# Optimization experiments

Measured on AMD Instinct MI355X. Metric: run time of the kernel, lower is better.

## Reference

```python
import jax, jax.numpy as jnp
import numpy as np
from jax import lax

SHIFT = 32  # shift_range from init
EPS_NORM = 1e-12
EPS_MASK = 1e-6


def _l2_normalize_flat(x):
    # F.normalize(x.reshape(B,-1)): per-sample L2 normalize with eps 1e-12
    B = x.shape[0]
    flat = x.reshape(B, -1)
    n = jnp.linalg.norm(flat, axis=1, keepdims=True)
    return (flat / jnp.maximum(n, EPS_NORM)).reshape(x.shape)


def setup_inputs() -> dict:
    key = jax.random.key(0)
    k1, k2 = jax.random.split(key)
    grd_feature = jax.random.normal(k1, (8, 32, 32, 32), dtype=jnp.float32)
    sat_feature = jax.random.normal(k2, (8, 32, 128, 128), dtype=jnp.float32)
    return {"grd_feature": grd_feature, "sat_feature": sat_feature, "test_method": 1}


def reference(grd_feature, sat_feature, test_method):
    # test_method == 1 path (default); test_method in {0,1} only differ in divisor
    M, C, H_s, W_s = sat_feature.shape
    N, _, H, W = grd_feature.shape
    kH = min(H, H_s - 2 * SHIFT)
    kW = min(W, W_s - 2 * SHIFT)

    # center-crop ground template to (kH, kW) and L2-normalize per sample
    gh0, gw0 = H // 2 - kH // 2, W // 2 - kW // 2
    grd = grd_feature[:, :, gh0:gh0 + 2 * (kH // 2), gw0:gw0 + 2 * (kW // 2)]
    N_, _, H_k, W_k = grd.shape
    grd = _l2_normalize_flat(grd)

    # center-crop satellite to search region and L2-normalize per sample
    sh0 = H_s // 2 - SHIFT - kH // 2
    sw0 = W_s // 2 - SHIFT - kW // 2
    sat = sat_feature[:, :, sh0:sh0 + 2 * (SHIFT + kH // 2), sw0:sw0 + 2 * (SHIFT + kW // 2)]
    _, _, H_i, W_i = sat.shape
    sat = _l2_normalize_flat(sat)

    # all-pairs cross-correlation: corr[m, n, y, x] (torch grouped-conv on repeated sat
    # is equivalent to a plain VALID conv of sat with all N ground filters)
    corr = lax.conv_general_dilated(
        sat, grd, window_strides=(1, 1), padding='VALID',
        dimension_numbers=('NCHW', 'OIHW', 'NCHW'))  # [M, N, Ho, Wo]
    Ho, Wo = corr.shape[2], corr.shape[3]

    # sliding-window sum of |sat|^2 (avg_pool with divisor_override=1, summed over C)
    s2 = jnp.sum(sat * sat, axis=1)  # [M, H_i, W_i]
    partical = lax.reduce_window(s2, jnp.float32(0), lax.add,
                                 (1, H_k, W_k), (1, 1, 1), 'VALID')  # [M, Ho, Wo]
    if test_method == 0:
        denom = jnp.sqrt(partical)
    else:
        denom = partical
    corr = corr / jnp.maximum(denom[:, None], EPS_NORM)

    similarity_matrix = jnp.max(corr, axis=(2, 3))  # [M, N]

    # diagonal pairs (m == n): peak localization
    diag = jnp.diagonal(corr, axis1=0, axis2=1)        # [Ho, Wo, M]
    diag = jnp.transpose(diag, (2, 0, 1)).reshape(M, -1)
    max_index = jnp.argmax(diag, axis=-1)
    pos_h = max_index // Wo
    pos_w = max_index % Wo

    grd_mask = (jnp.abs(jnp.sum(grd, axis=1)) > EPS_MASK).astype(jnp.float32)  # [N, H_k, W_k]

    def place(ph, pw, gm):
        z = jnp.zeros((1, H_i, W_i), dtype=jnp.float32)
        return lax.dynamic_update_slice(z, gm[None], (0, ph, pw))

    mask = jax.vmap(place)(pos_h, pos_w, grd_mask)  # [M, 1, H_i, W_i]
    return similarity_matrix, mask
```

## Files before the change

### kernel.cpp

```cpp
#include <hip/hip_runtime.h>
#include <stdint.h>

typedef unsigned short u16;
typedef unsigned int u32;
typedef unsigned long long u64;
typedef __bf16 bf16x8 __attribute__((ext_vector_type(8)));
typedef float floatx4 __attribute__((ext_vector_type(4)));

#define DEVI static __device__ __forceinline__

DEVI u16 f2bf(float f) {
  uint32_t u = __builtin_bit_cast(uint32_t, f);
  u += 0x7FFFu + ((u >> 16) & 1u);
  return (u16)(u >> 16);
}
DEVI float bf2f(u16 b) { return __builtin_bit_cast(float, (uint32_t)b << 16); }

DEVI u32 encf(float f) {
  u32 u = __builtin_bit_cast(u32, f);
  return (u >> 31) ? ~u : (u | 0x80000000u);
}

DEVI float wred_sum(float v) {
  #pragma unroll
  for (int o = 32; o > 0; o >>= 1) v += __shfl_xor(v, o);
  return v;
}
DEVI float wred_max(float v) {
  #pragma unroll
  for (int o = 32; o > 0; o >>= 1) v = fmaxf(v, __shfl_xor(v, o));
  return v;
}

DEVI void cp16(const u16* g, u16* l) {
#if __has_builtin(__builtin_amdgcn_global_load_lds)
  __builtin_amdgcn_global_load_lds(
      (const __attribute__((address_space(1))) uint32_t*)g,
      (__attribute__((address_space(3))) uint32_t*)l, 16, 0, 0);
#else
  *(uint4*)l = *(const uint4*)g;
#endif
}

static constexpr size_t OFF_CORRP = 0;
static constexpr size_t OFF_SATT  = OFF_CORRP + (size_t)4*270400*4;
static constexpr size_t OFF_GRDP  = OFF_SATT + (size_t)8*4*96*96*8*2;
static constexpr size_t OFF_S2    = OFF_GRDP + (size_t)4*1024*16*8*2;
static constexpr size_t OFF_PART  = OFF_S2   + (size_t)73728*4;
static constexpr size_t OFF_NRMP  = OFF_PART + (size_t)33800*4;
static constexpr size_t OFF_GNRM  = OFF_NRMP + 768*4;
static constexpr size_t OFF_MASK  = OFF_GNRM + 32;
static constexpr size_t OFF_PMAX  = OFF_MASK + (size_t)8192*4;
static constexpr size_t OFF_CNT   = OFF_PMAX + 320*4;
static constexpr size_t OFF_CAND  = OFF_CNT  + 512;

__global__ __launch_bounds__(256) void k_prep(
    const float* __restrict__ grd, const float* __restrict__ sat,
    u16* __restrict__ sTh, u16* __restrict__ gP,
    float* __restrict__ s2, float* __restrict__ nrmp,
    float* __restrict__ gnrm, float* __restrict__ gmask,
    u32* __restrict__ cnts) {
  __shared__ float L[32*100];
  __shared__ float red[4];
  const int t = threadIdx.x;
  if (blockIdx.x < 768) {
    const int m = blockIdx.x / 96, y = blockIdx.x - (blockIdx.x / 96) * 96;
    #pragma unroll
    for (int k = 0; k < 3; ++k) {
      const int idx = k*256 + t;
      const int c = idx / 24, xq = idx - c*24;
      const float4 v = *(const float4*)(sat + (((size_t)m*32 + c)*128 + (16+y))*128 + 16 + xq*4);
      *(float4*)(&L[c*100 + xq*4]) = v;
    }
    __syncthreads();
    float ss = 0.f;
    if (t < 96) {
      #pragma unroll
      for (int c = 0; c < 32; ++c) { const float v = L[c*100 + t]; ss += v*v; }
      s2[(size_t)m*9216 + y*96 + t] = ss;
    }
    const float wsum = wred_sum(ss);
    if ((t & 63) == 0) red[t >> 6] = wsum;
    __syncthreads();
    if (t == 0) nrmp[m*96 + y] = red[0] + red[1] + red[2] + red[3];
    for (int idx = t; idx < 384; idx += 256) {
      const int cb = idx / 96, x = idx - cb*96;
      union { u16 us[8]; uint4 v4; } P;
      #pragma unroll
      for (int e = 0; e < 8; ++e) P.us[e] = f2bf(L[(cb*8+e)*100 + x]);
      *(uint4*)(&sTh[(((size_t)m*4+cb)*9216 + (size_t)y*96 + x)*8]) = P.v4;
    }
  } else if (blockIdx.x == 776) {
    if (t < 96) cnts[t] = (t == 72) ? 768u : 0u;
  } else {
    const int n = blockIdx.x - 768;
    float nn = 0.f, scs[4];
    #pragma unroll
    for (int it = 0; it < 4; ++it) {
      const int pidx = it*256 + t;
      float vals[32]; float sc = 0.f;
      #pragma unroll
      for (int c = 0; c < 32; ++c) {
        const float v = grd[((size_t)n*32 + c)*1024 + pidx];
        vals[c] = v; sc += v; nn += v*v;
      }
      scs[it] = sc;
      #pragma unroll
      for (int cb = 0; cb < 4; ++cb) {
        union { u16 us[8]; uint4 v4; } ph, pl;
        #pragma unroll
        for (int e = 0; e < 8; ++e) {
          const float v = vals[cb*8+e];
          const u16 h = f2bf(v); ph.us[e] = h; pl.us[e] = f2bf(v - bf2f(h));
        }
        const size_t o = ((size_t)cb*1024 + pidx)*128;
        *(uint4*)(&gP[o + (size_t)n*8])     = ph.v4;
        *(uint4*)(&gP[o + (size_t)(n+8)*8]) = pl.v4;
      }
    }
    const float tot = wred_sum(nn);
    if ((t & 63) == 0) red[t >> 6] = tot;
    __syncthreads();
    const float sum = red[0] + red[1] + red[2] + red[3];
    if (t == 0) gnrm[n] = sum;
    const float gn = fmaxf(sqrtf(sum), 1e-12f);
    const float thr = 1e-6f * gn;
    #pragma unroll
    for (int it = 0; it < 4; ++it)
      gmask[n*1024 + it*256 + t] = (fabsf(scs[it]) > thr) ? 1.f : 0.f;
  }
}

__global__ __launch_bounds__(256, 3) void k_conv(
    const u16* __restrict__ satT, const u16* __restrict__ gP,
    const float* __restrict__ s2, float* __restrict__ corr_p,
    float* __restrict__ part, u32* __restrict__ tick)
{
  __shared__ __align__(16) u16 patch[41*48*8];
  __shared__ u32 s_bi;

  const int tid = threadIdx.x;
  const int wave = tid >> 6, lane = tid & 63;
  const int pr = lane & 15, q = lane >> 4;

  u32 bi = blockIdx.x;
  for (;;) {
    if (bi < 72) {
      float* S  = (float*)patch;
      float* HS = S + 40*96;
      const int pm = (int)bi / 9, ysl = ((int)bi - pm*9)*8;
      const int nrows = (65 - ysl) < 8 ? (65 - ysl) : 8;
      const int scnt  = (96 - ysl) < 40 ? (96 - ysl) : 40;
      for (int idx = tid; idx < scnt*96; idx += 256)
        S[idx] = s2[(size_t)pm*9216 + (size_t)ysl*96 + idx];
      __syncthreads();
      const int hrows = nrows + 31;
      for (int idx = tid; idx < hrows*65; idx += 256) {
        const int r = idx / 65, xo = idx - r*65;
        const float* p = &S[r*96 + xo];
        float s = 0.f;
        #pragma unroll
        for (int j = 0; j < 32; ++j) s += p[j];
        HS[idx] = s;
      }
      __syncthreads();
      for (int idx = tid; idx < nrows*65; idx += 256) {
        const int r = idx / 65, xo = idx - r*65;
        float s = 0.f;
        #pragma unroll
        for (int i = 0; i < 32; ++i) s += HS[(r+i)*65 + xo];
        part[(size_t)pm*4225 + (size_t)(ysl+r)*65 + xo] = s;
      }
    } else if (bi >= 968) {
      const int e = (int)bi - 968;
      const int cb = e & 3;
      const int yt = (e >> 2) % 5;
      const int m  = e / 20;
      const int ybase = yt * 13;
      const size_t rowbase = ((size_t)(m*4 + cb) * 96 + ybase) * 96;
      for (int k = tid; k < 44*32; k += 256) {
        const int rho = k >> 5, px = k & 31;
        cp16(&satT[(rowbase + (size_t)rho*96 + 64 + px)*8], &patch[(size_t)k*8]);
      }
      asm volatile("s_waitcnt vmcnt(0)" ::: "memory");
      __syncthreads();
      const int prc = pr < 13 ? pr : 12;
      floatx4 acc = (floatx4){0.f, 0.f, 0.f, 0.f};
      #pragma unroll
      for (int jbi = 0; jbi < 2; ++jbi) {
        const int jb = wave*2 + jbi;
        const int px_e = jb*4 + q;
        const u16* bp = gP + ((size_t)cb*1024 + (size_t)(jb*4+q))*128 + (size_t)pr*8;
        uint4 Br[8];
        #pragma unroll
        for (int ii = 0; ii < 8; ++ii) Br[ii] = *(const uint4*)(bp + (size_t)ii*4096);
        uint4 Ah[8];
        #pragma unroll
        for (int s = 0; s < 6; ++s)
          Ah[s] = *(const uint4*)(&patch[((size_t)(prc + s)*32 + px_e)*8]);
        #pragma unroll
        for (int i = 0; i < 32; ++i) {
          if (i < 26)
            Ah[(i+6)&7] = *(const uint4*)(&patch[((size_t)(prc + i + 6)*32 + px_e)*8]);
          const bf16x8 bf = __builtin_bit_cast(bf16x8, Br[i&7]);
          if (i < 24)
            Br[(i+8)&7] = *(const uint4*)(bp + (size_t)(i+8)*4096);
          acc = __builtin_amdgcn_mfma_f32_16x16x32_bf16(
              __builtin_bit_cast(bf16x8, Ah[i&7]), bf, acc, 0, 0, 0);
        }
      }
      float v4[4];
      #pragma unroll
      for (int k = 0; k < 4; ++k) v4[k] = acc[k] + __shfl_xor(acc[k], 8);
      __syncthreads();
      float* red = (float*)patch;
      #pragma unroll
      for (int k = 0; k < 4; ++k) red[((size_t)wave*64 + lane)*5 + k] = v4[k];
      __syncthreads();
      if (wave == 0 && pr < 8) {
        #pragma unroll
        for (int k = 0; k < 4; ++k) {
          const int yoff = q*4 + k;
          if (yoff < 13) {
            float s = 0.f;
            #pragma unroll
            for (int w = 0; w < 4; ++w) s += red[((size_t)w*64 + lane)*5 + k];
            corr_p[(size_t)cb*270400 + ((size_t)(m*8+pr)*65 + (ybase+yoff))*65 + 64] = s;
          }
        }
      }
    } else {
      int bb = (int)bi - 72;
      const int cb = bb & 3; bb >>= 2;
      const int xt = bb & 3; bb >>= 2;
      const int yt = bb % 7;
      const int m  = bb / 7;
      const int x0 = xt*16;

      if (yt < 6) {
        const int y0 = yt*10;
        const size_t rowbase = ((size_t)(m*4 + cb) * 96 + y0) * 96;
        for (int k = tid; k < 41*48; k += 256) {
          const int rho = k / 48, px = k - (k/48)*48;
          cp16(&satT[(rowbase + (size_t)rho*96 + x0 + px)*8], &patch[(size_t)k*8]);
        }
        asm volatile("s_waitcnt vmcnt(0)" ::: "memory");
        __syncthreads();

        floatx4 acc[10];
        #pragma unroll
        for (int r = 0; r < 10; ++r) acc[r] = (floatx4){0.f, 0.f, 0.f, 0.f};

        #pragma unroll
        for (int jbi = 0; jbi < 2; ++jbi) {
          const int jb = wave*2 + jbi;
          const int apx = pr + jb*4 + q;
          const u16* bp = gP + ((size_t)cb*1024 + (size_t)(jb*4+q))*128 + (size_t)pr*8;

          uint4 Br[8];
          #pragma unroll
          for (int ii = 0; ii < 8; ++ii) Br[ii] = *(const uint4*)(bp + (size_t)ii*4096);
          uint4 Ah[12];
          #pragma unroll
          for (int s = 0; s < 12; ++s) Ah[s] = *(const uint4*)(&patch[((size_t)s*48 + apx)*8]);

          #pragma unroll
          for (int i = 0; i < 32; ++i) {
            const bf16x8 bf = __builtin_bit_cast(bf16x8, Br[i&7]);
            if (i < 24)
              Br[(i+8)&7] = *(const uint4*)(bp + (size_t)(i+8)*4096);
            __builtin_amdgcn_s_setprio(1);
            #pragma unroll
            for (int r = 0; r < 10; ++r)
              acc[r] = __builtin_amdgcn_mfma_f32_16x16x32_bf16(
                  __builtin_bit_cast(bf16x8, Ah[(i+r)%12]), bf, acc[r], 0, 0, 0);
            __builtin_amdgcn_s_setprio(0);
            if (i < 29)
              Ah[(i+12)%12] = *(const uint4*)(&patch[((size_t)(i+12)*48 + apx)*8]);
          }
        }

        float* red = (float*)patch;
        #pragma unroll
        for (int half = 0; half < 2; ++half) {
          __syncthreads();
          #pragma unroll
          for (int u = 0; u < 20; ++u)
            red[((size_t)wave*64 + lane)*21 + u] = acc[half*5 + (u>>2)][u&3];
          __syncthreads();
          if (pr < 8) {
            const int fw = wave;
            #pragma unroll
            for (int r = 0; r < 5; ++r) {
              float s = 0.f;
              #pragma unroll
              for (int w = 0; w < 4; ++w)
                s += red[((size_t)w*64 + lane)*21 + r*4 + fw]
                   + red[((size_t)w*64 + (lane^8))*21 + r*4 + fw];
              const int x = x0 + q*4 + fw;
              corr_p[(size_t)cb*270400 + ((size_t)(m*8+pr)*65 + (y0 + half*5 + r))*65 + x] = s;
            }
          }
        }
      } else {
        const int y0 = 60;
        const size_t rowbase = ((size_t)(m*4 + cb) * 96 + y0) * 96;
        for (int k = tid; k < 36*48; k += 256) {
          const int rho = k / 48, px = k - (k/48)*48;
          cp16(&satT[(rowbase + (size_t)rho*96 + x0 + px)*8], &patch[(size_t)k*8]);
        }
        asm volatile("s_waitcnt vmcnt(0)" ::: "memory");
        __syncthreads();

        floatx4 acc[5];
        #pragma unroll
        for (int r = 0; r < 5; ++r) acc[r] = (floatx4){0.f, 0.f, 0.f, 0.f};

        #pragma unroll
        for (int jbi = 0; jbi < 2; ++jbi) {
          const int jb = wave*2 + jbi;
          const int apx = pr + jb*4 + q;
          const u16* bp = gP + ((size_t)cb*1024 + (size_t)(jb*4+q))*128 + (size_t)pr*8;

          uint4 Br[8];
          #pragma unroll
          for (int ii = 0; ii < 8; ++ii) Br[ii] = *(const uint4*)(bp + (size_t)ii*4096);
          uint4 Ah[8];
          #pragma unroll
          for (int s = 0; s < 6; ++s) Ah[s] = *(const uint4*)(&patch[((size_t)s*48 + apx)*8]);

          #pragma unroll
          for (int i = 0; i < 32; ++i) {
            if (i < 30)
              Ah[(i+6)&7] = *(const uint4*)(&patch[((size_t)(i+6)*48 + apx)*8]);
            const bf16x8 bf = __builtin_bit_cast(bf16x8, Br[i&7]);
            if (i < 24)
              Br[(i+8)&7] = *(const uint4*)(bp + (size_t)(i+8)*4096);
            __builtin_amdgcn_s_setprio(1);
            #pragma unroll
            for (int r = 0; r < 5; ++r)
              acc[r] = __builtin_amdgcn_mfma_f32_16x16x32_bf16(
                  __builtin_bit_cast(bf16x8, Ah[(i+r)&7]), bf, acc[r], 0, 0, 0);
            __builtin_amdgcn_s_setprio(0);
          }
        }

        __syncthreads();
        float* red = (float*)patch;
        #pragma unroll
        for (int u = 0; u < 20; ++u)
          red[((size_t)wave*64 + lane)*21 + u] = acc[u>>2][u&3];
        __syncthreads();
        if (pr < 8) {
          const int fw = wave;
          #pragma unroll
          for (int r = 0; r < 5; ++r) {
            float s = 0.f;
            #pragma unroll
            for (int w = 0; w < 4; ++w)
              s += red[((size_t)w*64 + lane)*21 + r*4 + fw]
                 + red[((size_t)w*64 + (lane^8))*21 + r*4 + fw];
            const int x = x0 + q*4 + fw;
            corr_p[(size_t)cb*270400 + ((size_t)(m*8+pr)*65 + (y0+r))*65 + x] = s;
          }
        }
      }
    }

    __syncthreads();
    if (tid == 0) s_bi = atomicAdd(tick, 1u);
    __syncthreads();
    bi = s_bi;
    if (bi >= 1128) return;
  }
}

__global__ __launch_bounds__(256) void k_post(
    const float* __restrict__ corr_p, const float* __restrict__ part,
    const float* __restrict__ nrmp, const float* __restrict__ gnrm,
    const int* __restrict__ tm,
    u32* __restrict__ pmaxE, u32* __restrict__ grpcnt,
    u32* __restrict__ candcnt, u64* __restrict__ cand,
    float* __restrict__ out)
{
  __shared__ float red[8];
  __shared__ int s_last;

  const int bi = blockIdx.x;
  const int m = bi / 40, n = (bi / 5) & 7, yc = bi % 5, g = m*8 + n;
  const int t = threadIdx.x;
  const int wv = t >> 6, ln = t & 63;
  const bool diag = (m == n);

  float v0 = (t < 96) ? nrmp[m*96 + t] : 0.f;
  v0 = wred_sum(v0);
  if (ln == 0) red[wv] = v0;
  __syncthreads();
  const float snrm2 = red[0] + red[1] + red[2] + red[3];
  const float srn = 1.f / fmaxf(sqrtf(snrm2), 1e-12f);
  const float grn = 1.f / fmaxf(sqrtf(gnrm[n]), 1e-12f);
  const float cscale = grn * srn, pscale = srn * srn;
  const int method = tm[0];

  const float* cp = corr_p + (size_t)g*4225;
  const float* pp = part + (size_t)m*4225;
  const int i0 = yc*845, i1 = i0 + 845;
  float vv[4];
  float bestv = -3.4e38f;
  #pragma unroll
  for (int k = 0; k < 4; ++k) {
    const int idx = i0 + k*256 + t;
    float v = -3.4e38f;
    if (idx < i1) {
      const float c = cp[idx] + cp[idx+270400] + cp[idx+540800] + cp[idx+811200];
      const float pt = pp[idx] * pscale;
      float denom = (method == 0) ? sqrtf(pt) : pt;
      denom = fmaxf(denom, 1e-12f);
      v = c * cscale / denom;
    }
    vv[k] = v;
    bestv = fmaxf(bestv, v);
  }
  __syncthreads();
  const float bw = wred_max(bestv);
  if (ln == 0) red[wv] = bw;
  __syncthreads();
  const float bmax = fmaxf(fmaxf(red[0], red[1]), fmaxf(red[2], red[3]));
  if (t == 0) atomicExch(&pmaxE[bi], encf(bmax));

  if (diag) {
    const float lthr = bmax - 3e-3f;
    #pragma unroll
    for (int k = 0; k < 4; ++k) {
      const int idx = i0 + k*256 + t;
      if (idx < i1 && vv[k] >= lthr) {
        const u32 s = atomicAdd(&candcnt[n], 1u);
        if (s < 128)
          atomicExch(&cand[n*128 + s],
                     ((u64)__builtin_bit_cast(u32, vv[k]) << 32) | (u32)idx);
      }
    }
  }
  __syncthreads();
  if (t == 0) s_last = (atomicAdd(&grpcnt[g], 1u) == 4u) ? 1 : 0;
  __syncthreads();
  if (!s_last) return;

  if (t < 5) red[t] = __builtin_bit_cast(float, 0u);
  if (t < 5) {
    const u32 e = atomicOr(&pmaxE[g*5 + t], 0u);
    const u32 u = (e >> 31) ? (e & 0x7FFFFFFFu) : ~e;
    red[t] = __builtin_bit_cast(float, u);
  }
  __syncthreads();
  const float gmax = fmaxf(fmaxf(fmaxf(red[0], red[1]), fmaxf(red[2], red[3])), red[4]);
  if (t == 0) out[g] = gmax;
}

__global__ __launch_bounds__(256) void k_refine(
    const float* __restrict__ part, const float* __restrict__ nrmp,
    const float* __restrict__ gnrm, const int* __restrict__ tm,
    const float* __restrict__ grd, const float* __restrict__ sat,
    const float* __restrict__ gmask,
    const u32* __restrict__ candcnt, const u64* __restrict__ cand,
    float* __restrict__ out)
{
  __shared__ float red[4];
  __shared__ int fidx[128];
  __shared__ u32 fcnt;
  __shared__ u64 wkey[4];

  const int n = blockIdx.x;
  const int t = threadIdx.x;
  const int wv = t >> 6, ln = t & 63;

  float v0 = (t < 96) ? nrmp[n*96 + t] : 0.f;
  v0 = wred_sum(v0);
  if (ln == 0) red[wv] = v0;
  if (t == 0) fcnt = 0u;
  __syncthreads();
  const float snrm2 = red[0] + red[1] + red[2] + red[3];
  const float srn = 1.f / fmaxf(sqrtf(snrm2), 1e-12f);
  const float grn = 1.f / fmaxf(sqrtf(gnrm[n]), 1e-12f);
  const float cscale = grn * srn, pscale = srn * srn;
  const int method = tm[0];

  const float gmax = out[9*n];
  const float thr = gmax - 3e-3f;

  u32 nc = candcnt[n]; if (nc > 128u) nc = 128u;
  if (t < (int)nc) {
    const u64 pk = cand[n*128 + t];
    const float vf = __builtin_bit_cast(float, (u32)(pk >> 32));
    const int idx = (int)(u32)pk;
    if (vf >= thr) {
      const u32 s = atomicAdd(&fcnt, 1u);
      if (s < 128u) fidx[s] = idx;
    }
  }
  __syncthreads();
  if (t == 0 && fcnt == 0u) { fidx[0] = 0; fcnt = 1u; }
  __syncthreads();
  const int nf = (int)(fcnt < 128u ? fcnt : 128u);

  u64 bestKey = 0ULL;
  for (int ci = wv; ci < nf; ci += 4) {
    const int idx = fidx[ci];
    const int y = idx / 65, x = idx - y*65;
    float a = 0.f;
    #pragma unroll
    for (int k = 0; k < 16; ++k) {
      const int p = ln + 64*k;
      const int c = p >> 5, i = p & 31;
      const float4* gr4 = (const float4*)(grd + ((size_t)n*32 + c)*1024 + i*32);
      const float* sr = sat + (((size_t)n*32 + c)*128 + (16 + y + i))*128 + (16 + x);
      #pragma unroll
      for (int j4 = 0; j4 < 8; ++j4) {
        const float4 g4 = gr4[j4];
        a += g4.x*sr[j4*4] + g4.y*sr[j4*4+1] + g4.z*sr[j4*4+2] + g4.w*sr[j4*4+3];
      }
    }
    a = wred_sum(a);
    if (ln == 0) {
      const float pt = part[(size_t)n*4225 + idx] * pscale;
      float denom = (method == 0) ? sqrtf(pt) : pt;
      denom = fmaxf(denom, 1e-12f);
      const float v = a * cscale / denom;
      const u64 key = ((u64)encf(v) << 32) | (u64)(0xFFFFFFFFu - (u32)idx);
      if (key > bestKey) bestKey = key;
    }
  }
  if (ln == 0) wkey[wv] = bestKey;
  __syncthreads();
  u64 bk = wkey[0];
  if (wkey[1] > bk) bk = wkey[1];
  if (wkey[2] > bk) bk = wkey[2];
  if (wkey[3] > bk) bk = wkey[3];
  const int bix = (int)(0xFFFFFFFFu - (u32)bk);
  const int ph = bix / 65, pw = bix - (bix/65)*65;
  for (int p = t; p < 9216; p += 256) {
    const int yy = p / 96, xx = p - yy*96;
    float val = 0.f;
    if (yy >= ph && yy < ph+32 && xx >= pw && xx < pw+32)
      val = gmask[n*1024 + (yy-ph)*32 + (xx-pw)];
    out[64 + (size_t)n*9216 + p] = val;
  }
}

extern "C" void kernel_launch(void* const* d_in, const int* in_sizes, int n_in,
                              void* d_out, int out_size, void* d_ws, size_t ws_size,
                              hipStream_t stream) {
  const float* grd = (const float*)d_in[0];
  const float* sat = (const float*)d_in[1];
  const int*   tm  = (const int*)d_in[2];
  float* out = (float*)d_out;
  char* ws = (char*)d_ws;

  float* corrp = (float*)(ws + OFF_CORRP);
  u16*   sTh   = (u16*)(ws + OFF_SATT);
  u16*   gP    = (u16*)(ws + OFF_GRDP);
  float* s2    = (float*)(ws + OFF_S2);
  float* part  = (float*)(ws + OFF_PART);
  float* nrmp  = (float*)(ws + OFF_NRMP);
  float* gnrm  = (float*)(ws + OFF_GNRM);
  float* gmask = (float*)(ws + OFF_MASK);
  u32*   pmaxE = (u32*)(ws + OFF_PMAX);
  u32*   cnts  = (u32*)(ws + OFF_CNT);
  u32*   candcnt = cnts + 64;
  u32*   tick  = cnts + 72;
  u64*   cand  = (u64*)(ws + OFF_CAND);

  k_prep<<<777, 256, 0, stream>>>(grd, sat, sTh, gP, s2, nrmp, gnrm, gmask, cnts);
  k_conv<<<768, 256, 0, stream>>>(sTh, gP, s2, corrp, part, tick);
  k_post<<<320, 256, 0, stream>>>(corrp, part, nrmp, gnrm, tm,
                                  pmaxE, cnts, candcnt, cand, out);
  k_refine<<<8, 256, 0, stream>>>(part, nrmp, gnrm, tm, grd, sat, gmask,
                                  candcnt, cand, out);
}
```

Before: 158.7 us.

## Parallelize refine across candidates with per-candidate blocks and atomic max

```diff
diff --git a/kernel.cpp b/kernel.cpp
--- a/kernel.cpp
+++ b/kernel.cpp
@@ -91,7 +91,9 @@
       *(uint4*)(&sTh[(((size_t)m*4+cb)*9216 + (size_t)y*96 + x)*8]) = P.v4;
     }
   } else if (blockIdx.x == 776) {
-    if (t < 96) cnts[t] = (t == 72) ? 768u : 0u;
+    if (t < 112)
+      cnts[t] = (t == 72) ? 768u
+              : ((t >= 96 && !(t & 1)) ? 0xFFFFFFFFu : 0u);
   } else {
     const int n = blockIdx.x - 768;
     float nn = 0.f, scs[4];
@@ -381,6 +383,7 @@
     const int* __restrict__ tm,
     u32* __restrict__ pmaxE, u32* __restrict__ grpcnt,
     u32* __restrict__ candcnt, u64* __restrict__ cand,
+    float* __restrict__ cscN, float* __restrict__ pscN,
     float* __restrict__ out)
 {
   __shared__ float red[8];
@@ -401,6 +404,7 @@
   const float grn = 1.f / fmaxf(sqrtf(gnrm[n]), 1e-12f);
   const float cscale = grn * srn, pscale = srn * srn;
   const int method = tm[0];
+  if (diag && t == 0) { cscN[n] = cscale; pscN[n] = pscale; }
 
   const float* cp = corr_p + (size_t)g*4225;
   const float* pp = part + (size_t)m*4225;
@@ -446,7 +450,6 @@
   __syncthreads();
   if (!s_last) return;
 
-  if (t < 5) red[t] = __builtin_bit_cast(float, 0u);
   if (t < 5) {
     const u32 e = atomicOr(&pmaxE[g*5 + t], 0u);
     const u32 u = (e >> 31) ? (e & 0x7FFFFFFFu) : ~e;
@@ -458,84 +461,63 @@
 }
 
 __global__ __launch_bounds__(256) void k_refine(
-    const float* __restrict__ part, const float* __restrict__ nrmp,
-    const float* __restrict__ gnrm, const int* __restrict__ tm,
+    const float* __restrict__ part, const int* __restrict__ tm,
     const float* __restrict__ grd, const float* __restrict__ sat,
     const float* __restrict__ gmask,
     const u32* __restrict__ candcnt, const u64* __restrict__ cand,
+    const float* __restrict__ cscN, const float* __restrict__ pscN,
+    u32* __restrict__ rdone, u64* __restrict__ bestu,
     float* __restrict__ out)
 {
   __shared__ float red[4];
-  __shared__ int fidx[128];
-  __shared__ u32 fcnt;
-  __shared__ u64 wkey[4];
-
-  const int n = blockIdx.x;
+  __shared__ int s_last;
+
+  const int bid = blockIdx.x;
+  const int n = bid >> 7, ci = bid & 127;
   const int t = threadIdx.x;
   const int wv = t >> 6, ln = t & 63;
 
-  float v0 = (t < 96) ? nrmp[n*96 + t] : 0.f;
-  v0 = wred_sum(v0);
-  if (ln == 0) red[wv] = v0;
-  if (t == 0) fcnt = 0u;
-  __syncthreads();
-  const float snrm2 = red[0] + red[1] + red[2] + red[3];
-  const float srn = 1.f / fmaxf(sqrtf(snrm2), 1e-12f);
-  const float grn = 1.f / fmaxf(sqrtf(gnrm[n]), 1e-12f);
-  const float cscale = grn * srn, pscale = srn * srn;
-  const int method = tm[0];
-
-  const float gmax = out[9*n];
-  const float thr = gmax - 3e-3f;
-
   u32 nc = candcnt[n]; if (nc > 128u) nc = 128u;
-  if (t < (int)nc) {
-    const u64 pk = cand[n*128 + t];
+  bool act = (ci < (int)nc);
+  int idx = 0;
+  if (act) {
+    const u64 pk = cand[n*128 + ci];
     const float vf = __builtin_bit_cast(float, (u32)(pk >> 32));
-    const int idx = (int)(u32)pk;
-    if (vf >= thr) {
-      const u32 s = atomicAdd(&fcnt, 1u);
-      if (s < 128u) fidx[s] = idx;
-    }
-  }
-  __syncthreads();
-  if (t == 0 && fcnt == 0u) { fidx[0] = 0; fcnt = 1u; }
-  __syncthreads();
-  const int nf = (int)(fcnt < 128u ? fcnt : 128u);
-
-  u64 bestKey = 0ULL;
-  for (int ci = wv; ci < nf; ci += 4) {
-    const int idx = fidx[ci];
+    idx = (int)(u32)pk;
+    act = (vf >= out[9*n] - 3e-3f);
+  }
+  if (act) {
     const int y = idx / 65, x = idx - y*65;
+    const int i0 = t >> 5, j = t & 31;
+    const float* gb = grd + (size_t)n*32768 + i0*32 + j;
+    const float* sb = sat + (((size_t)n*32*128) + 16 + y + i0)*128 + 16 + x + j;
     float a = 0.f;
-    #pragma unroll
-    for (int k = 0; k < 16; ++k) {
-      const int p = ln + 64*k;
-      const int c = p >> 5, i = p & 31;
-      const float4* gr4 = (const float4*)(grd + ((size_t)n*32 + c)*1024 + i*32);
-      const float* sr = sat + (((size_t)n*32 + c)*128 + (16 + y + i))*128 + (16 + x);
-      #pragma unroll
-      for (int j4 = 0; j4 < 8; ++j4) {
-        const float4 g4 = gr4[j4];
-        a += g4.x*sr[j4*4] + g4.y*sr[j4*4+1] + g4.z*sr[j4*4+2] + g4.w*sr[j4*4+3];
-      }
+    #pragma unroll 4
+    for (int c = 0; c < 32; ++c) {
+      #pragma unroll
+      for (int ii = 0; ii < 4; ++ii)
+        a += gb[(size_t)(c*32 + ii*8)*32] * sb[((size_t)c*128 + ii*8)*128];
     }
     a = wred_sum(a);
-    if (ln == 0) {
-      const float pt = part[(size_t)n*4225 + idx] * pscale;
-      float denom = (method == 0) ? sqrtf(pt) : pt;
+    if (ln == 0) red[wv] = a;
+    __syncthreads();
+    if (t == 0) {
+      const float tot = red[0] + red[1] + red[2] + red[3];
+      const float pt = part[(size_t)n*4225 + idx] * pscN[n];
+      float denom = (tm[0] == 0) ? sqrtf(pt) : pt;
       denom = fmaxf(denom, 1e-12f);
-      const float v = a * cscale / denom;
+      const float v = tot * cscN[n] / denom;
       const u64 key = ((u64)encf(v) << 32) | (u64)(0xFFFFFFFFu - (u32)idx);
-      if (key > bestKey) bestKey = key;
-    }
-  }
-  if (ln == 0) wkey[wv] = bestKey;
-  __syncthreads();
-  u64 bk = wkey[0];
-  if (wkey[1] > bk) bk = wkey[1];
-  if (wkey[2] > bk) bk = wkey[2];
-  if (wkey[3] > bk) bk = wkey[3];
+      atomicMax(&bestu[n], key);
+    }
+  }
+  __threadfence();
+  __syncthreads();
+  if (t == 0) s_last = (atomicAdd(&rdone[n], 1u) == 127u) ? 1 : 0;
+  __syncthreads();
+  if (!s_last) return;
+
+  const u64 bk = atomicAdd(&bestu[n], 0ULL);
   const int bix = (int)(0xFFFFFFFFu - (u32)bk);
   const int ph = bix / 65, pw = bix - (bix/65)*65;
   for (int p = t; p < 9216; p += 256) {
@@ -568,12 +550,17 @@
   u32*   cnts  = (u32*)(ws + OFF_CNT);
   u32*   candcnt = cnts + 64;
   u32*   tick  = cnts + 72;
+  u32*   rdone = cnts + 88;
+  u64*   bestu = (u64*)(ws + OFF_CNT + 384);
+  float* cscN  = (float*)(cnts + 112);
+  float* pscN  = (float*)(cnts + 120);
   u64*   cand  = (u64*)(ws + OFF_CAND);
 
   k_prep<<<777, 256, 0, stream>>>(grd, sat, sTh, gP, s2, nrmp, gnrm, gmask, cnts);
   k_conv<<<768, 256, 0, stream>>>(sTh, gP, s2, corrp, part, tick);
   k_post<<<320, 256, 0, stream>>>(corrp, part, nrmp, gnrm, tm,
-                                  pmaxE, cnts, candcnt, cand, out);
-  k_refine<<<8, 256, 0, stream>>>(part, nrmp, gnrm, tm, grd, sat, gmask,
-                                  candcnt, cand, out);
-}
+                                  pmaxE, cnts, candcnt, cand, cscN, pscN, out);
+  k_refine<<<1024, 256, 0, stream>>>(part, tm, grd, sat, gmask,
+                                     candcnt, cand, cscN, pscN,
+                                     rdone, bestu, out);
+}
```

Result: slower. 189.5 us (+19.3%).
